# Performance work log

Measured on AMD Instinct MI355X. Metric: run time of the kernel, lower is better.

The kernel has to match this reference:

```python
import jax, jax.numpy as jnp
import numpy as np

PATCH_SIZE = [3, 5, 7]
PATCH_SEQ = [5, 7]
SEQ_SIZE = 6
WIN = 210
D_MODEL = 256
B, M = 8, 55
EPS = 1e-5


def _loo(p):
    # leave-one-out index matrix, row i = all indices except i -> (p, p-1)
    return np.array([[k for k in range(p) if k != i] for i in range(p)], dtype=np.int32)


def _mlp(x, W1, b1, W2, b2):
    # torch MLP: fc2(relu(fc1(x))), Linear weights are (out, in)
    h = jax.nn.relu(x @ W1.T + b1)
    return h @ W2.T + b2


def _forward(x, sP, nP, ssP, nsP):
    Bn, L, Mn = x.shape
    # RevIN 'norm' with fresh affine (weight=1, bias=0): identity affine; stats detached
    mean = jax.lax.stop_gradient(jnp.mean(x, axis=1, keepdims=True))
    std = jax.lax.stop_gradient(jnp.sqrt(jnp.var(x, axis=1, keepdims=True) + EPS))
    xn = (x - mean) / std
    xt = jnp.transpose(xn, (0, 2, 1)).reshape(Bn * Mn, L)  # (BM, L)
    sm, pm, ssr, psr = [], [], [], []
    for j, p in enumerate(PATCH_SIZE):
        n = L // p
        x3 = xt.reshape(Bn * Mn, p, n)  # l = r*n + k
        # size branch: leave-one-out over the p axis, blocks ordered i*n + k
        feat = jnp.transpose(x3[:, _loo(p), :], (0, 1, 3, 2)).reshape(Bn * Mn, L, p - 1)
        y = _mlp(feat, *sP[j])[..., 0]  # (BM, L)
        sm.append(jnp.transpose(y.reshape(Bn, Mn, L), (0, 2, 1)))
        # num branch: leave-one-out over the n axis of row l%p, leaving out column l//p
        g = _mlp(x3[:, :, _loo(n)], *nP[j])[..., 0]  # (BM, p, n)
        # torch cats over l (axis 0) then reshapes (B, M, L): flat order is (l, b, m)
        prior = jnp.transpose(g, (2, 1, 0)).reshape(Bn, Mn, L)  # faithful scrambled reshape
        pm.append(jnp.transpose(prior, (0, 2, 1)))
    s = SEQ_SIZE
    for j, p in enumerate(PATCH_SEQ):
        n = L // (p * s)
        x4 = xt.reshape(Bn * Mn, p, n, s)  # l = (r*n + k)*s + t
        # size_seq branch: leave-one-out over p, feature = (p-1)*s per (i, k) position
        feat = jnp.transpose(x4[:, _loo(p)], (0, 1, 3, 2, 4)).reshape(Bn * Mn, p * n, (p - 1) * s)
        y = _mlp(feat, *ssP[j])  # (BM, p*n, s)
        ssr.append(jnp.transpose(y.reshape(Bn, Mn, L), (0, 2, 1)))
        # num_seq branch: leave-one-out over n, cat order i*p + r
        featn = jnp.transpose(x4[:, :, _loo(n), :], (0, 2, 1, 3, 4)).reshape(Bn * Mn, n * p, (n - 1) * s)
        g = _mlp(featn, *nsP[j])  # (BM, n*p, s)
        d0 = PATCH_SEQ[0]  # original code hardcodes patch_seq[0] here
        h = jnp.transpose(g.reshape(Bn, Mn, (n * p) // d0, d0, s), (0, 1, 3, 2, 4)).reshape(Bn, Mn, L)
        psr.append(jnp.transpose(h, (0, 2, 1)))
    # original returns 4 lists of (B, L, M); stack all 10 for a single output
    return jnp.stack(sm + pm + ssr + psr, axis=0)


def setup_inputs() -> dict:
    key = jax.random.key(0)
    keys = iter(jax.random.split(key, 128))
    d = {"x": jax.random.normal(next(keys), (B, WIN, M), dtype=jnp.float32)}

    def lin(name, out_d, in_d):
        d[name + "W"] = jax.random.normal(next(keys), (out_d, in_d), dtype=jnp.float32) / np.float32(np.sqrt(in_d))
        d[name + "b"] = jax.random.normal(next(keys), (out_d,), dtype=jnp.float32) * np.float32(0.01)

    for j, p in enumerate(PATCH_SIZE):
        lin(f"s1_{j}", D_MODEL, p - 1)
        lin(f"s2_{j}", 1, D_MODEL)
        lin(f"n1_{j}", D_MODEL, WIN // p - 1)
        lin(f"n2_{j}", 1, D_MODEL)
    for j, p in enumerate(PATCH_SEQ):
        lin(f"ss1_{j}", D_MODEL, (p - 1) * SEQ_SIZE)
        lin(f"ss2_{j}", SEQ_SIZE, D_MODEL)
        lin(f"ns1_{j}", D_MODEL, WIN // p - SEQ_SIZE)
        lin(f"ns2_{j}", SEQ_SIZE, D_MODEL)
    return d


def reference(x, s1_0W, s1_0b, s2_0W, s2_0b, n1_0W, n1_0b, n2_0W, n2_0b,
              s1_1W, s1_1b, s2_1W, s2_1b, n1_1W, n1_1b, n2_1W, n2_1b,
              s1_2W, s1_2b, s2_2W, s2_2b, n1_2W, n1_2b, n2_2W, n2_2b,
              ss1_0W, ss1_0b, ss2_0W, ss2_0b, ns1_0W, ns1_0b, ns2_0W, ns2_0b,
              ss1_1W, ss1_1b, ss2_1W, ss2_1b, ns1_1W, ns1_1b, ns2_1W, ns2_1b):
    sP = [(s1_0W, s1_0b, s2_0W, s2_0b), (s1_1W, s1_1b, s2_1W, s2_1b), (s1_2W, s1_2b, s2_2W, s2_2b)]
    nP = [(n1_0W, n1_0b, n2_0W, n2_0b), (n1_1W, n1_1b, n2_1W, n2_1b), (n1_2W, n1_2b, n2_2W, n2_2b)]
    ssP = [(ss1_0W, ss1_0b, ss2_0W, ss2_0b), (ss1_1W, ss1_1b, ss2_1W, ss2_1b)]
    nsP = [(ns1_0W, ns1_0b, ns2_0W, ns2_0b), (ns1_1W, ns1_1b, ns2_1W, ns2_1b)]
    return _forward(x, sP, nP, ssP, nsP)
```

## Files before the change

### kernel.cpp

```cpp
#include <hip/hip_runtime.h>

#define LL  210
#define MM  55
#define NBM 440
#define DM  256
#define MLT 11550
#define BLM 92400

#define XTG_OFF  0
#define W1T_OFF  92400
#define REC_OFF  158704

__device__ __forceinline__ float wave_sum(float v) {
#pragma unroll
    for (int off = 32; off > 0; off >>= 1) v += __shfl_xor(v, off, 64);
    return v;
}

__device__ __forceinline__ void fma4(float4& a, const float4 w, const float s) {
    a.x += w.x * s; a.y += w.y * s; a.z += w.z * s; a.w += w.w * s;
}
__device__ __forceinline__ void fms4(float4& a, const float4 w, const float s) {
    a.x -= w.x * s; a.y -= w.y * s; a.z -= w.z * s; a.w -= w.w * s;
}

__device__ __forceinline__ float bfly8(const float y[8], const int lane) {
    float z[4];
#pragma unroll
    for (int i = 0; i < 4; ++i) {
        float snd = (lane & 1) ? y[2*i] : y[2*i+1];
        float rcv = __shfl_xor(snd, 1, 64);
        z[i] = ((lane & 1) ? y[2*i+1] : y[2*i]) + rcv;
    }
    float u[2];
#pragma unroll
    for (int i = 0; i < 2; ++i) {
        float snd = (lane & 2) ? z[2*i] : z[2*i+1];
        float rcv = __shfl_xor(snd, 2, 64);
        u[i] = ((lane & 2) ? z[2*i+1] : z[2*i]) + rcv;
    }
    {
        float snd = (lane & 4) ? u[0] : u[1];
        float rcv = __shfl_xor(snd, 4, 64);
        float w = ((lane & 4) ? u[1] : u[0]) + rcv;
        w += __shfl_xor(w, 8, 64);
        w += __shfl_xor(w, 16, 64);
        w += __shfl_xor(w, 32, 64);
        return w;
    }
}

__global__ __launch_bounds__(256) void knorm_trans(
        const float* __restrict__ x,
        const float* __restrict__ nw0, const float* __restrict__ nw1, const float* __restrict__ nw2,
        const float* __restrict__ ssw0, const float* __restrict__ ssw1,
        const float* __restrict__ nsw0, const float* __restrict__ nsw1,
        const float* __restrict__ s1W0, const float* __restrict__ s1b0, const float* __restrict__ s2W0,
        const float* __restrict__ s1W1, const float* __restrict__ s1b1, const float* __restrict__ s2W1,
        const float* __restrict__ s1W2, const float* __restrict__ s1b2, const float* __restrict__ s2W2,
        float* __restrict__ xtg, float* __restrict__ w1t, float* __restrict__ recs) {
    __shared__ float red[8];
    const int t = threadIdx.x;
    const int blk = blockIdx.x;
    if (blk < NBM) {
        const int bm = blk, b = bm / MM, m = bm % MM;
        const int wid = t >> 6, lane = t & 63;
        float v = (t < LL) ? x[b * MLT + t * MM + m] : 0.f;
        float s1 = wave_sum(v);
        float s2 = wave_sum(v * v);
        if (lane == 0) { red[wid] = s1; red[4 + wid] = s2; }
        __syncthreads();
        float mean = (red[0] + red[1] + red[2] + red[3]) * (1.f / 210.f);
        float msq  = (red[4] + red[5] + red[6] + red[7]) * (1.f / 210.f);
        float var = msq - mean * mean;
        float inv = rsqrtf(var + 1e-5f);
        if (t < LL) xtg[(bm >> 3) * 1680 + t * 8 + (bm & 7)] = (v - mean) * inv;
    } else if (blk < NBM + 259) {
        const int e = (blk - NBM) * 256 + t;
        const int cg = e >> 8, d = e & 255;
        const float* src; int ind, c;
        if (cg < 69)       { src = nw0;  ind = 69; c = cg; }
        else if (cg < 110) { src = nw1;  ind = 41; c = cg - 69; }
        else if (cg < 139) { src = nw2;  ind = 29; c = cg - 110; }
        else if (cg < 163) { src = ssw0; ind = 24; c = cg - 139; }
        else if (cg < 199) { src = ssw1; ind = 36; c = cg - 163; }
        else if (cg < 235) { src = nsw0; ind = 36; c = cg - 199; }
        else               { src = nsw1; ind = 24; c = cg - 235; }
        w1t[cg * DM + d] = src[d * ind + c];
    } else {
        const int e = (blk - NBM - 259) * 256 + t;
        float v;
        if (e < 1024) {
            int d = e >> 2, c = e & 3;
            v = (c < 2) ? s1W0[d * 2 + c] : (c == 2 ? s1b0[d] : s2W0[d]);
        } else if (e < 3072) {
            int rel = e - 1024, d = rel >> 3, c = rel & 7;
            v = (c < 4) ? s1W1[d * 4 + c] : (c == 4 ? s1b1[d] : (c == 5 ? s2W1[d] : 0.f));
        } else {
            int rel = e - 3072, d = rel >> 3, c = rel & 7;
            v = (c < 6) ? s1W2[d * 6 + c] : (c == 6 ? s1b2[d] : s2W2[d]);
        }
        recs[e] = v;
    }
}

template <int IND>
__device__ __forceinline__ void ksize_body(const float* __restrict__ xtg,
        const float* __restrict__ rec, const float* __restrict__ b2,
        int bm, int j, float* __restrict__ out) {
    constexpr int N = LL / (IND + 1);
    const int t = threadIdx.x;
    if (t >= LL) return;
    const float* xs = xtg + (bm >> 3) * 1680 + (bm & 7);
    const int i = t / N, k = t - i * N;
    float f[IND];
#pragma unroll
    for (int idx = 0; idx < IND; ++idx) {
        int row = idx + (idx >= i);
        f[idx] = xs[(row * N + k) * 8];
    }
    float y0 = b2[0], y1 = 0.f;
    const float4* r4 = (const float4*)rec;
    if constexpr (IND == 2) {
#pragma unroll 8
        for (int d = 0; d < DM; d += 2) {
            const float4 a = r4[d], b = r4[d + 1];
            y0 += fmaxf(a.x * f[0] + a.y * f[1] + a.z, 0.f) * a.w;
            y1 += fmaxf(b.x * f[0] + b.y * f[1] + b.z, 0.f) * b.w;
        }
    } else if constexpr (IND == 4) {
#pragma unroll 8
        for (int d = 0; d < DM; d += 2) {
            const float4 a = r4[2*d], b = r4[2*d+1];
            const float4 c = r4[2*d+2], e = r4[2*d+3];
            y0 += fmaxf(a.x*f[0] + a.y*f[1] + a.z*f[2] + a.w*f[3] + b.x, 0.f) * b.y;
            y1 += fmaxf(c.x*f[0] + c.y*f[1] + c.z*f[2] + c.w*f[3] + e.x, 0.f) * e.y;
        }
    } else {
#pragma unroll 8
        for (int d = 0; d < DM; d += 2) {
            const float4 a = r4[2*d], b = r4[2*d+1];
            const float4 c = r4[2*d+2], e = r4[2*d+3];
            y0 += fmaxf(a.x*f[0] + a.y*f[1] + a.z*f[2] + a.w*f[3] + b.x*f[4] + b.y*f[5] + b.z, 0.f) * b.w;
            y1 += fmaxf(c.x*f[0] + c.y*f[1] + c.z*f[2] + c.w*f[3] + e.x*f[4] + e.y*f[5] + e.z, 0.f) * e.w;
        }
    }
    const int b_ = bm / MM, m = bm - b_ * MM;
    out[j * BLM + b_ * MLT + t * MM + m] = y0 + y1;
}

template <int P, int N>
__device__ __forceinline__ void knum_body(const float* __restrict__ xtg,
        const float* __restrict__ wt, const float* __restrict__ b1,
        const float* __restrict__ W2, const float* __restrict__ b2,
        int grp, int r, int j, float* __restrict__ out) {
    const int t = threadIdx.x, wid = t >> 6, lane = t & 63;
    const int g0 = wid * 2;
    const float* xb = xtg + grp * 1680 + r * N * 8 + g0;
    const float4 b1v = *(const float4*)&b1[lane * 4];
    const float4 w2v = *(const float4*)&W2[lane * 4];
    const float b2v = b2[0];
    const float* wl = wt + lane * 4;
    float4 A0 = b1v, A1 = b1v;
    float4 B0 = make_float4(0.f,0.f,0.f,0.f), B1 = B0;
#pragma unroll 2
    for (int q = 1; q < N; ++q) {
        const float4 w = *(const float4*)(wl + (q - 1) * DM);
        const float2 xv = *(const float2*)(xb + q * 8);
        fma4(B0, w, xv.x); fma4(B1, w, xv.y);
    }
    constexpr int NFULL = N / 8, TAIL = N - NFULL * 8;
    for (int c = 0; c <= NFULL; ++c) {
        float y0[8], y1[8];
        const bool full = (c < NFULL);
#pragma unroll
        for (int i = 0; i < 8; ++i) {
            const int k = c * 8 + i;
            if (full || i < TAIL) {
                float hx = fmaxf(A0.x + B0.x, 0.f), hy = fmaxf(A0.y + B0.y, 0.f);
                float hz = fmaxf(A0.z + B0.z, 0.f), hw = fmaxf(A0.w + B0.w, 0.f);
                y0[i] = hx * w2v.x + hy * w2v.y + hz * w2v.z + hw * w2v.w;
                hx = fmaxf(A1.x + B1.x, 0.f); hy = fmaxf(A1.y + B1.y, 0.f);
                hz = fmaxf(A1.z + B1.z, 0.f); hw = fmaxf(A1.w + B1.w, 0.f);
                y1[i] = hx * w2v.x + hy * w2v.y + hz * w2v.z + hw * w2v.w;
                if (full || i < TAIL - 1) {
                    const float4 w = *(const float4*)(wl + k * DM);
                    const float2 xk  = *(const float2*)(xb + k * 8);
                    const float2 xk1 = *(const float2*)(xb + k * 8 + 8);
                    fma4(A0, w, xk.x);  fma4(A1, w, xk.y);
                    fms4(B0, w, xk1.x); fms4(B1, w, xk1.y);
                }
            } else { y0[i] = 0.f; y1[i] = 0.f; }
        }
        const float v0 = bfly8(y0, lane), v1 = bfly8(y1, lane);
        if (lane < 16) {
            const int k = c * 8 + (lane & 7);
            if (k < N) {
                const int bm = grp * 8 + g0 + (lane >> 3);
                const float val = ((lane < 8) ? v0 : v1) + b2v;
                const int fi = (k * P + r) * NBM + bm;
                const int ob = fi / MLT, rem = fi - ob * MLT;
                const int om = rem / LL, ol = rem - om * LL;
                out[(3 + j) * BLM + ob * MLT + ol * MM + om] = val;
            }
        }
    }
}

template <int ISNUM, int P, int N>
__device__ __forceinline__ void kseq_body(const float* __restrict__ xtg,
        const float* __restrict__ w1tb, const float* __restrict__ b1,
        const float* __restrict__ W2, const float* __restrict__ b2,
        int grp, int qc, int slab, float* __restrict__ out) {
    constexpr int NROWS = ISNUM ? (N - 1) : (P - 1);
    const int t = threadIdx.x, wid = t >> 6, lane = t & 63;
    const float4 b1v = *(const float4*)&b1[lane * 4];
    const float* xg = xtg + grp * 1680;
    float b2r[6];
#pragma unroll
    for (int tt = 0; tt < 6; ++tt) b2r[tt] = b2[tt];
    const int bm = grp * 8 + (lane & 7);
    const int b_ = bm / MM, m = bm - b_ * MM;
    const int qe = (qc * 9 + 9 < 35) ? (qc * 9 + 9) : 35;
    for (int q = qc * 9 + wid; q < qe; q += 4) {
        int pivot, fix;
        if (ISNUM) { pivot = q / P; fix = q - pivot * P; }
        else       { pivot = q / N; fix = q - pivot * N; }
        float4 acc[8];
#pragma unroll
        for (int g = 0; g < 8; ++g) acc[g] = b1v;
        const float* wl = w1tb + lane * 4;
        for (int idx = 0; idx < NROWS; ++idx) {
            const int row = idx + (idx >= pivot);
            const int pos0 = ISNUM ? (fix * N + row) * 6 : (row * N + fix) * 6;
            const float* xp = xg + pos0 * 8;
#pragma unroll
            for (int tt = 0; tt < 6; ++tt) {
                const float4 xa = *(const float4*)(xp + tt * 8);
                const float4 xc = *(const float4*)(xp + tt * 8 + 4);
                const float4 w  = *(const float4*)wl; wl += DM;
                fma4(acc[0], w, xa.x); fma4(acc[1], w, xa.y);
                fma4(acc[2], w, xa.z); fma4(acc[3], w, xa.w);
                fma4(acc[4], w, xc.x); fma4(acc[5], w, xc.y);
                fma4(acc[6], w, xc.z); fma4(acc[7], w, xc.w);
            }
        }
#pragma unroll
        for (int g = 0; g < 8; ++g) {
            acc[g].x = fmaxf(acc[g].x, 0.f); acc[g].y = fmaxf(acc[g].y, 0.f);
            acc[g].z = fmaxf(acc[g].z, 0.f); acc[g].w = fmaxf(acc[g].w, 0.f);
        }
        const int c2 = q / 5, dd = q - c2 * 5;
#pragma unroll
        for (int h = 0; h < 2; ++h) {
            float yv0[8], yv1[8], yv2[8];
#pragma unroll
            for (int tt2 = 0; tt2 < 3; ++tt2) {
                const int tt = h * 3 + tt2;
                const float4 w2v = *(const float4*)&W2[tt * DM + lane * 4];
                float* yv = (tt2 == 0) ? yv0 : ((tt2 == 1) ? yv1 : yv2);
#pragma unroll
                for (int g = 0; g < 8; ++g)
                    yv[g] = acc[g].x * w2v.x + acc[g].y * w2v.y + acc[g].z * w2v.z + acc[g].w * w2v.w;
            }
            const float r0 = bfly8(yv0, lane);
            const float r1 = bfly8(yv1, lane);
            const float r2 = bfly8(yv2, lane);
            if (lane < 8) {
#pragma unroll
                for (int tt2 = 0; tt2 < 3; ++tt2) {
                    const int tt = h * 3 + tt2;
                    const int l = ISNUM ? (dd * 42 + c2 * 6 + tt) : (q * 6 + tt);
                    const float rv = (tt2 == 0) ? r0 : ((tt2 == 1) ? r1 : r2);
                    out[slab + b_ * MLT + l * MM + m] = rv + b2r[tt];
                }
            }
        }
    }
}

__global__ __launch_bounds__(256) void kfused(const float* __restrict__ xtg,
        const float* __restrict__ w1t, const float* __restrict__ recs,
        const float* __restrict__ b2s0, const float* __restrict__ b2s1, const float* __restrict__ b2s2,
        const float* __restrict__ nb1_0, const float* __restrict__ nW2_0, const float* __restrict__ nb2_0,
        const float* __restrict__ nb1_1, const float* __restrict__ nW2_1, const float* __restrict__ nb2_1,
        const float* __restrict__ nb1_2, const float* __restrict__ nW2_2, const float* __restrict__ nb2_2,
        const float* __restrict__ ss1b0, const float* __restrict__ ss2W0, const float* __restrict__ ss2b0,
        const float* __restrict__ ss1b1, const float* __restrict__ ss2W1, const float* __restrict__ ss2b1,
        const float* __restrict__ ns1b0, const float* __restrict__ ns2W0, const float* __restrict__ ns2b0,
        const float* __restrict__ ns1b1, const float* __restrict__ ns2W1, const float* __restrict__ ns2b1,
        float* __restrict__ out) {
    const int blk = blockIdx.x;
    if (blk < 1320) {
        if (blk < NBM)          ksize_body<2>(xtg, recs,        b2s0, blk,           0, out);
        else if (blk < 2 * NBM) ksize_body<4>(xtg, recs + 1024, b2s1, blk - NBM,     1, out);
        else                    ksize_body<6>(xtg, recs + 3072, b2s2, blk - 2 * NBM, 2, out);
    } else if (blk < 2145) {
        const int bn = blk - 1320;
        if (bn < 165) {
            int rel = bn;       knum_body<3, 70>(xtg, w1t,            nb1_0, nW2_0, nb2_0, rel / 3, rel % 3, 0, out);
        } else if (bn < 440) {
            int rel = bn - 165; knum_body<5, 42>(xtg, w1t + 69 * DM,  nb1_1, nW2_1, nb2_1, rel / 5, rel % 5, 1, out);
        } else {
            int rel = bn - 440; knum_body<7, 30>(xtg, w1t + 110 * DM, nb1_2, nW2_2, nb2_2, rel / 7, rel % 7, 2, out);
        }
    } else {
        const int bs = blk - 2145;
        const int tc = bs / 220, rem = bs - tc * 220;
        const int grp = rem >> 2, qc = rem & 3;
        if (tc == 0)      kseq_body<0, 5, 7>(xtg, w1t + 139 * DM, ss1b0, ss2W0, ss2b0, grp, qc, 6 * BLM, out);
        else if (tc == 1) kseq_body<0, 7, 5>(xtg, w1t + 163 * DM, ss1b1, ss2W1, ss2b1, grp, qc, 7 * BLM, out);
        else if (tc == 2) kseq_body<1, 5, 7>(xtg, w1t + 199 * DM, ns1b0, ns2W0, ns2b0, grp, qc, 8 * BLM, out);
        else              kseq_body<1, 7, 5>(xtg, w1t + 235 * DM, ns1b1, ns2W1, ns2b1, grp, qc, 9 * BLM, out);
    }
}

extern "C" void kernel_launch(void* const* d_in, const int* in_sizes, int n_in,
                              void* d_out, int out_size, void* d_ws, size_t ws_size,
                              hipStream_t stream) {
    (void)in_sizes; (void)n_in; (void)out_size; (void)ws_size;
    const float* x = (const float*)d_in[0];
    const float *s1W[3], *s1b[3], *s2W[3], *s2b[3], *n1W[3], *n1b[3], *n2W[3], *n2b[3];
    for (int j = 0; j < 3; ++j) {
        int base = 1 + j * 8;
        s1W[j] = (const float*)d_in[base + 0]; s1b[j] = (const float*)d_in[base + 1];
        s2W[j] = (const float*)d_in[base + 2]; s2b[j] = (const float*)d_in[base + 3];
        n1W[j] = (const float*)d_in[base + 4]; n1b[j] = (const float*)d_in[base + 5];
        n2W[j] = (const float*)d_in[base + 6]; n2b[j] = (const float*)d_in[base + 7];
    }
    const float *ss1W[2], *ss1b[2], *ss2W[2], *ss2b[2], *ns1W[2], *ns1b[2], *ns2W[2], *ns2b[2];
    for (int j = 0; j < 2; ++j) {
        int base = 25 + j * 8;
        ss1W[j] = (const float*)d_in[base + 0]; ss1b[j] = (const float*)d_in[base + 1];
        ss2W[j] = (const float*)d_in[base + 2]; ss2b[j] = (const float*)d_in[base + 3];
        ns1W[j] = (const float*)d_in[base + 4]; ns1b[j] = (const float*)d_in[base + 5];
        ns2W[j] = (const float*)d_in[base + 6]; ns2b[j] = (const float*)d_in[base + 7];
    }
    float* out  = (float*)d_out;
    float* xtg  = (float*)d_ws + XTG_OFF;
    float* w1t  = (float*)d_ws + W1T_OFF;
    float* recs = (float*)d_ws + REC_OFF;

    knorm_trans<<<719, 256, 0, stream>>>(x,
        n1W[0], n1W[1], n1W[2],
        ss1W[0], ss1W[1], ns1W[0], ns1W[1],
        s1W[0], s1b[0], s2W[0],
        s1W[1], s1b[1], s2W[1],
        s1W[2], s1b[2], s2W[2],
        xtg, w1t, recs);
    kfused<<<3025, 256, 0, stream>>>(xtg, w1t, recs,
        s2b[0], s2b[1], s2b[2],
        n1b[0], n2W[0], n2b[0],
        n1b[1], n2W[1], n2b[1],
        n1b[2], n2W[2], n2b[2],
        ss1b[0], ss2W[0], ss2b[0],
        ss1b[1], ss2W[1], ss2b[1],
        ns1b[0], ns2W[0], ns2b[0],
        ns1b[1], ns2W[1], ns2b[1], out);
}
```

Measured before the change: 222.9 us.

## Batch size-branch over two series, coalesce norm prep, permute block order

Each size-branch block now processes two adjacent (b,m) series, so every recorded weight loaded from memory feeds twice the arithmetic and the size-branch block count halves. The normalisation prep handles 8 series per block, giving coalesced reads of x and cutting prep blocks from 440 to 55. The fused kernel's block index is permuted (multiplied by 997 mod 2365) to interleave heavy and light branch blocks across the GPU, and one loop's unroll factor rises. In exchange there is more register pressure in the size body, fewer size-branch blocks to spread across CUs, and the permutation relies on 997 being coprime with 2365.

```diff
diff --git a/kernel.cpp b/kernel.cpp
--- a/kernel.cpp
+++ b/kernel.cpp
@@ -10,12 +10,6 @@
 #define XTG_OFF  0
 #define W1T_OFF  92400
 #define REC_OFF  158704
-
-__device__ __forceinline__ float wave_sum(float v) {
-#pragma unroll
-    for (int off = 32; off > 0; off >>= 1) v += __shfl_xor(v, off, 64);
-    return v;
-}
 
 __device__ __forceinline__ void fma4(float4& a, const float4 w, const float s) {
     a.x += w.x * s; a.y += w.y * s; a.z += w.z * s; a.w += w.w * s;
@@ -50,7 +44,7 @@
     }
 }
 
-__global__ __launch_bounds__(256) void knorm_trans(
+__global__ __launch_bounds__(256) void kprep(
         const float* __restrict__ x,
         const float* __restrict__ nw0, const float* __restrict__ nw1, const float* __restrict__ nw2,
         const float* __restrict__ ssw0, const float* __restrict__ ssw1,
@@ -59,24 +53,39 @@
         const float* __restrict__ s1W1, const float* __restrict__ s1b1, const float* __restrict__ s2W1,
         const float* __restrict__ s1W2, const float* __restrict__ s1b2, const float* __restrict__ s2W2,
         float* __restrict__ xtg, float* __restrict__ w1t, float* __restrict__ recs) {
-    __shared__ float red[8];
     const int t = threadIdx.x;
     const int blk = blockIdx.x;
-    if (blk < NBM) {
-        const int bm = blk, b = bm / MM, m = bm % MM;
+    if (blk < 55) {
+        const int mi = t & 7, li = t >> 3;
+        const int bm = blk * 8 + mi;
+        const int b = bm / MM, m = bm - b * MM;
+        const float* xp = x + b * MLT + m;
+        float vr[7], s1 = 0.f, s2 = 0.f;
+#pragma unroll
+        for (int it = 0; it < 7; ++it) {
+            const int l = li + 32 * it;
+            const float v = (l < LL) ? xp[l * MM] : 0.f;
+            vr[it] = v; s1 += v; s2 += v * v;
+        }
+        s1 += __shfl_xor(s1, 8, 64);  s2 += __shfl_xor(s2, 8, 64);
+        s1 += __shfl_xor(s1, 16, 64); s2 += __shfl_xor(s2, 16, 64);
+        s1 += __shfl_xor(s1, 32, 64); s2 += __shfl_xor(s2, 32, 64);
+        __shared__ float red[2][4][8];
         const int wid = t >> 6, lane = t & 63;
-        float v = (t < LL) ? x[b * MLT + t * MM + m] : 0.f;
-        float s1 = wave_sum(v);
-        float s2 = wave_sum(v * v);
-        if (lane == 0) { red[wid] = s1; red[4 + wid] = s2; }
+        if (lane < 8) { red[0][wid][lane] = s1; red[1][wid][lane] = s2; }
         __syncthreads();
-        float mean = (red[0] + red[1] + red[2] + red[3]) * (1.f / 210.f);
-        float msq  = (red[4] + red[5] + red[6] + red[7]) * (1.f / 210.f);
-        float var = msq - mean * mean;
-        float inv = rsqrtf(var + 1e-5f);
-        if (t < LL) xtg[(bm >> 3) * 1680 + t * 8 + (bm & 7)] = (v - mean) * inv;
-    } else if (blk < NBM + 259) {
-        const int e = (blk - NBM) * 256 + t;
+        const float S1 = red[0][0][mi] + red[0][1][mi] + red[0][2][mi] + red[0][3][mi];
+        const float S2 = red[1][0][mi] + red[1][1][mi] + red[1][2][mi] + red[1][3][mi];
+        const float mean = S1 * (1.f / 210.f);
+        const float inv = rsqrtf(S2 * (1.f / 210.f) - mean * mean + 1e-5f);
+        float* xo = xtg + blk * 1680 + mi;
+#pragma unroll
+        for (int it = 0; it < 7; ++it) {
+            const int l = li + 32 * it;
+            if (l < LL) xo[l * 8] = (vr[it] - mean) * inv;
+        }
+    } else if (blk < 55 + 259) {
+        const int e = (blk - 55) * 256 + t;
         const int cg = e >> 8, d = e & 255;
         const float* src; int ind, c;
         if (cg < 69)       { src = nw0;  ind = 69; c = cg; }
@@ -88,7 +97,7 @@
         else               { src = nsw1; ind = 24; c = cg - 235; }
         w1t[cg * DM + d] = src[d * ind + c];
     } else {
-        const int e = (blk - NBM - 259) * 256 + t;
+        const int e = (blk - 55 - 259) * 256 + t;
         float v;
         if (e < 1024) {
             int d = e >> 2, c = e & 3;
@@ -105,48 +114,60 @@
 }
 
 template <int IND>
-__device__ __forceinline__ void ksize_body(const float* __restrict__ xtg,
+__device__ __forceinline__ void ksize_body2(const float* __restrict__ xtg,
         const float* __restrict__ rec, const float* __restrict__ b2,
-        int bm, int j, float* __restrict__ out) {
+        int bm0, int j, float* __restrict__ out) {
     constexpr int N = LL / (IND + 1);
     const int t = threadIdx.x;
     if (t >= LL) return;
-    const float* xs = xtg + (bm >> 3) * 1680 + (bm & 7);
+    const float* xs = xtg + (bm0 >> 3) * 1680 + (bm0 & 7);
     const int i = t / N, k = t - i * N;
-    float f[IND];
+    float2 f[IND];
 #pragma unroll
     for (int idx = 0; idx < IND; ++idx) {
-        int row = idx + (idx >= i);
-        f[idx] = xs[(row * N + k) * 8];
-    }
-    float y0 = b2[0], y1 = 0.f;
+        const int row = idx + (idx >= i);
+        f[idx] = *(const float2*)&xs[(row * N + k) * 8];
+    }
+    const float b2v = b2[0];
+    float y0a = 0.f, y0b = 0.f, y1a = 0.f, y1b = 0.f;
     const float4* r4 = (const float4*)rec;
     if constexpr (IND == 2) {
 #pragma unroll 8
         for (int d = 0; d < DM; d += 2) {
             const float4 a = r4[d], b = r4[d + 1];
-            y0 += fmaxf(a.x * f[0] + a.y * f[1] + a.z, 0.f) * a.w;
-            y1 += fmaxf(b.x * f[0] + b.y * f[1] + b.z, 0.f) * b.w;
+            y0a += fmaxf(a.x * f[0].x + a.y * f[1].x + a.z, 0.f) * a.w;
+            y1a += fmaxf(a.x * f[0].y + a.y * f[1].y + a.z, 0.f) * a.w;
+            y0b += fmaxf(b.x * f[0].x + b.y * f[1].x + b.z, 0.f) * b.w;
+            y1b += fmaxf(b.x * f[0].y + b.y * f[1].y + b.z, 0.f) * b.w;
         }
     } else if constexpr (IND == 4) {
 #pragma unroll 8
         for (int d = 0; d < DM; d += 2) {
             const float4 a = r4[2*d], b = r4[2*d+1];
             const float4 c = r4[2*d+2], e = r4[2*d+3];
-            y0 += fmaxf(a.x*f[0] + a.y*f[1] + a.z*f[2] + a.w*f[3] + b.x, 0.f) * b.y;
-            y1 += fmaxf(c.x*f[0] + c.y*f[1] + c.z*f[2] + c.w*f[3] + e.x, 0.f) * e.y;
+            y0a += fmaxf(a.x*f[0].x + a.y*f[1].x + a.z*f[2].x + a.w*f[3].x + b.x, 0.f) * b.y;
+            y1a += fmaxf(a.x*f[0].y + a.y*f[1].y + a.z*f[2].y + a.w*f[3].y + b.x, 0.f) * b.y;
+            y0b += fmaxf(c.x*f[0].x + c.y*f[1].x + c.z*f[2].x + c.w*f[3].x + e.x, 0.f) * e.y;
+            y1b += fmaxf(c.x*f[0].y + c.y*f[1].y + c.z*f[2].y + c.w*f[3].y + e.x, 0.f) * e.y;
         }
     } else {
 #pragma unroll 8
         for (int d = 0; d < DM; d += 2) {
             const float4 a = r4[2*d], b = r4[2*d+1];
             const float4 c = r4[2*d+2], e = r4[2*d+3];
-            y0 += fmaxf(a.x*f[0] + a.y*f[1] + a.z*f[2] + a.w*f[3] + b.x*f[4] + b.y*f[5] + b.z, 0.f) * b.w;
-            y1 += fmaxf(c.x*f[0] + c.y*f[1] + c.z*f[2] + c.w*f[3] + e.x*f[4] + e.y*f[5] + e.z, 0.f) * e.w;
-        }
-    }
-    const int b_ = bm / MM, m = bm - b_ * MM;
-    out[j * BLM + b_ * MLT + t * MM + m] = y0 + y1;
+            y0a += fmaxf(a.x*f[0].x + a.y*f[1].x + a.z*f[2].x + a.w*f[3].x + b.x*f[4].x + b.y*f[5].x + b.z, 0.f) * b.w;
+            y1a += fmaxf(a.x*f[0].y + a.y*f[1].y + a.z*f[2].y + a.w*f[3].y + b.x*f[4].y + b.y*f[5].y + b.z, 0.f) * b.w;
+            y0b += fmaxf(c.x*f[0].x + c.y*f[1].x + c.z*f[2].x + c.w*f[3].x + e.x*f[4].x + e.y*f[5].x + e.z, 0.f) * e.w;
+            y1b += fmaxf(c.x*f[0].y + c.y*f[1].y + c.z*f[2].y + c.w*f[3].y + e.x*f[4].y + e.y*f[5].y + e.z, 0.f) * e.w;
+        }
+    }
+#pragma unroll
+    for (int g = 0; g < 2; ++g) {
+        const int bm = bm0 + g;
+        const int b_ = bm / MM, m = bm - b_ * MM;
+        const float y = (g ? (y1a + y1b) : (y0a + y0b)) + b2v;
+        out[j * BLM + b_ * MLT + t * MM + m] = y;
+    }
 }
 
 template <int P, int N>
@@ -163,7 +184,7 @@
     const float* wl = wt + lane * 4;
     float4 A0 = b1v, A1 = b1v;
     float4 B0 = make_float4(0.f,0.f,0.f,0.f), B1 = B0;
-#pragma unroll 2
+#pragma unroll 4
     for (int q = 1; q < N; ++q) {
         const float4 w = *(const float4*)(wl + (q - 1) * DM);
         const float2 xv = *(const float2*)(xb + q * 8);
@@ -290,13 +311,15 @@
         const float* __restrict__ ns1b0, const float* __restrict__ ns2W0, const float* __restrict__ ns2b0,
         const float* __restrict__ ns1b1, const float* __restrict__ ns2W1, const float* __restrict__ ns2b1,
         float* __restrict__ out) {
-    const int blk = blockIdx.x;
-    if (blk < 1320) {
-        if (blk < NBM)          ksize_body<2>(xtg, recs,        b2s0, blk,           0, out);
-        else if (blk < 2 * NBM) ksize_body<4>(xtg, recs + 1024, b2s1, blk - NBM,     1, out);
-        else                    ksize_body<6>(xtg, recs + 3072, b2s2, blk - 2 * NBM, 2, out);
-    } else if (blk < 2145) {
-        const int bn = blk - 1320;
+    const int blk = (int)(((unsigned)blockIdx.x * 997u) % 2365u);
+    if (blk < 660) {
+        const int j = blk / 220, rel = blk - j * 220;
+        const int bm0 = rel * 2;
+        if (j == 0)      ksize_body2<2>(xtg, recs,        b2s0, bm0, 0, out);
+        else if (j == 1) ksize_body2<4>(xtg, recs + 1024, b2s1, bm0, 1, out);
+        else             ksize_body2<6>(xtg, recs + 3072, b2s2, bm0, 2, out);
+    } else if (blk < 1485) {
+        const int bn = blk - 660;
         if (bn < 165) {
             int rel = bn;       knum_body<3, 70>(xtg, w1t,            nb1_0, nW2_0, nb2_0, rel / 3, rel % 3, 0, out);
         } else if (bn < 440) {
@@ -305,7 +328,7 @@
             int rel = bn - 440; knum_body<7, 30>(xtg, w1t + 110 * DM, nb1_2, nW2_2, nb2_2, rel / 7, rel % 7, 2, out);
         }
     } else {
-        const int bs = blk - 2145;
+        const int bs = blk - 1485;
         const int tc = bs / 220, rem = bs - tc * 220;
         const int grp = rem >> 2, qc = rem & 3;
         if (tc == 0)      kseq_body<0, 5, 7>(xtg, w1t + 139 * DM, ss1b0, ss2W0, ss2b0, grp, qc, 6 * BLM, out);
@@ -341,14 +364,14 @@
     float* w1t  = (float*)d_ws + W1T_OFF;
     float* recs = (float*)d_ws + REC_OFF;
 
-    knorm_trans<<<719, 256, 0, stream>>>(x,
+    kprep<<<334, 256, 0, stream>>>(x,
         n1W[0], n1W[1], n1W[2],
         ss1W[0], ss1W[1], ns1W[0], ns1W[1],
         s1W[0], s1b[0], s2W[0],
         s1W[1], s1b[1], s2W[1],
         s1W[2], s1b[2], s2W[2],
         xtg, w1t, recs);
-    kfused<<<3025, 256, 0, stream>>>(xtg, w1t, recs,
+    kfused<<<2365, 256, 0, stream>>>(xtg, w1t, recs,
         s2b[0], s2b[1], s2b[2],
         n1b[0], n2W[0], n2b[0],
         n1b[1], n2W[1], n2b[1],
```

New measurement: 229.2 us. 2.9% more time.
